# Kernel tuning notes

Measured on AMD Instinct MI355X. Metric: run time of the kernel, lower is better.

Reference implementation:

```python
import jax, jax.numpy as jnp
import numpy as np

_KX = jnp.array([[1., 0., -1.], [2., 0., -2.], [1., 0., -1.]], dtype=jnp.float32).reshape(1, 1, 3, 3)
_KY = jnp.transpose(_KX, (0, 1, 3, 2))  # ky = kx.transpose(2,3)


def _sobel(x, k):
    # x: [B,1,H,W], k: [1,1,3,3]; SAME padding=1, stride 1
    return jax.lax.conv_general_dilated(
        x, k, window_strides=(1, 1), padding=((1, 1), (1, 1)),
        dimension_numbers=('NCHW', 'OIHW', 'NCHW'))


def setup_inputs() -> dict:
    key = jax.random.key(0)
    k1, k2 = jax.random.split(key)
    sr = jax.random.normal(k1, (32, 1, 1024, 1024), dtype=jnp.float32)
    hr = jax.random.normal(k2, (32, 1, 1024, 1024), dtype=jnp.float32)
    return {"sr": sr, "hr": hr}


def reference(sr, hr):
    gx_sr = _sobel(sr, _KX)
    gy_sr = _sobel(sr, _KY)
    gx_hr = _sobel(hr, _KX)
    gy_hr = _sobel(hr, _KY)
    return jnp.mean(jnp.abs(gx_sr - gx_hr) + jnp.abs(gy_sr - gy_hr))
```

## Files before the change

### kernel.cpp

```cpp
#include <hip/hip_runtime.h>


#define IMG_H 1024
#define IMG_W 1024
#define IMG_B 32
#define CH 8
#define NROW (CH + 2)
#define NCHUNK (IMG_H / CH)

#define GLOBAL_PTR(p) ((const __attribute__((address_space(1))) void*)(p))
#define LDS_PTR(p)    ((__attribute__((address_space(3))) void*)(p))

__device__ __forceinline__ void row_st_lds(const float* __restrict__ a,
                                           const float* __restrict__ b,
                                           int x0, float m,
                                           float4& s, float4& t) {
    const float4 av = *reinterpret_cast<const float4*>(a + x0);
    const float4 bv = *reinterpret_cast<const float4*>(b + x0);
    float4 d;
    d.x = (av.x - bv.x) * m;
    d.y = (av.y - bv.y) * m;
    d.z = (av.z - bv.z) * m;
    d.w = (av.w - bv.w) * m;
    const float dl = (x0 > 0)           ? (a[x0 - 1] - b[x0 - 1]) * m : 0.f;
    const float dr = (x0 + 4 < IMG_W)   ? (a[x0 + 4] - b[x0 + 4]) * m : 0.f;
    s.x = dl  + 2.f * d.x + d.y;
    s.y = d.x + 2.f * d.y + d.z;
    s.z = d.y + 2.f * d.z + d.w;
    s.w = d.z + 2.f * d.w + dr;
    t.x = dl  - d.y;
    t.y = d.x - d.z;
    t.z = d.y - d.w;
    t.w = d.z - dr;
}

__global__ __launch_bounds__(256) void edge_loss_kernel(
        const float* __restrict__ sr, const float* __restrict__ hr,
        float* __restrict__ out, float invN) {
    __shared__ __align__(16) float lA[NROW][IMG_W];
    __shared__ __align__(16) float lB[NROW][IMG_W];

    const int chunk = blockIdx.x;
    const int b     = blockIdx.y;
    const int tid   = threadIdx.x;
    const int lane  = tid & 63;
    const int wave  = tid >> 6;
    const int x0    = tid * 4;
    const int wseg  = wave * 256;
    const size_t img = (size_t)b * IMG_H * IMG_W;
    const int y0 = chunk * CH;

    #pragma unroll
    for (int r = 0; r < NROW; ++r) {
        const int yc = min(max(y0 - 1 + r, 0), IMG_H - 1);
        const size_t off = img + (size_t)yc * IMG_W + wseg + lane * 4;
        __builtin_amdgcn_global_load_lds(GLOBAL_PTR(sr + off), LDS_PTR(&lA[r][wseg]), 16, 0, 0);
        __builtin_amdgcn_global_load_lds(GLOBAL_PTR(hr + off), LDS_PTR(&lB[r][wseg]), 16, 0, 0);
    }
    __syncthreads();

    const float mtop = (y0 > 0) ? 1.f : 0.f;
    const float mbot = (y0 + CH < IMG_H) ? 1.f : 0.f;

    float4 s0, t0, s1, t1, s2, t2;
    row_st_lds(lA[0], lB[0], x0, mtop, s0, t0);
    row_st_lds(lA[1], lB[1], x0, 1.f,  s1, t1);

    float acc = 0.f;
    #pragma unroll
    for (int i = 2; i < NROW; ++i) {
        const float m = (i == NROW - 1) ? mbot : 1.f;
        row_st_lds(lA[i], lB[i], x0, m, s2, t2);

        float gx, gy;
        gx = t0.x + 2.f * t1.x + t2.x;  gy = s0.x - s2.x;  acc += fabsf(gx) + fabsf(gy);
        gx = t0.y + 2.f * t1.y + t2.y;  gy = s0.y - s2.y;  acc += fabsf(gx) + fabsf(gy);
        gx = t0.z + 2.f * t1.z + t2.z;  gy = s0.z - s2.z;  acc += fabsf(gx) + fabsf(gy);
        gx = t0.w + 2.f * t1.w + t2.w;  gy = s0.w - s2.w;  acc += fabsf(gx) + fabsf(gy);

        s0 = s1; t0 = t1; s1 = s2; t1 = t2;
    }

    #pragma unroll
    for (int off = 32; off > 0; off >>= 1)
        acc += __shfl_down(acc, off, 64);

    __syncthreads();
    if (lane == 0) lA[0][wave] = acc;
    __syncthreads();
    if (tid == 0) {
        const float bsum = lA[0][0] + lA[0][1] + lA[0][2] + lA[0][3];
        atomicAdd(out, bsum * invN);
    }
}

extern "C" void kernel_launch(void* const* d_in, const int* in_sizes, int n_in,
                              void* d_out, int out_size, void* d_ws, size_t ws_size,
                              hipStream_t stream) {
    const float* sr = (const float*)d_in[0];
    const float* hr = (const float*)d_in[1];
    float* out = (float*)d_out;

    hipMemsetAsync(out, 0, sizeof(float), stream);

    dim3 grid(NCHUNK, IMG_B);
    const float invN = 1.0f / (float)((size_t)IMG_B * IMG_H * IMG_W);
    edge_loss_kernel<<<grid, 256, 0, stream>>>(sr, hr, out, invN);
}
```

Before: 278.3 us.

## Process 64-row strips per block with an LDS ring buffer and prefetching

Each block now handles a 64-row strip in eight 8-row chunks instead of a single chunk. An 18-row LDS ring is filled with global_load_lds, and the next chunk's rows are prefetched while the current one is computed, synchronised with vmcnt waits and barriers. This removes the halo re-reads between chunks and overlaps load latency with compute. In exchange it uses 144KB of LDS per block, allowing about one block per CU, and launches far fewer blocks (512), which risks lower occupancy and idle CUs.

```diff
diff --git a/kernel.cpp b/kernel.cpp
--- a/kernel.cpp
+++ b/kernel.cpp
@@ -5,8 +5,9 @@
 #define IMG_W 1024
 #define IMG_B 32
 #define CH 8
-#define NROW (CH + 2)
-#define NCHUNK (IMG_H / CH)
+#define NCHUNK 8
+#define STRIPS (IMG_H / (CH * NCHUNK))
+#define RING 18
 
 #define GLOBAL_PTR(p) ((const __attribute__((address_space(1))) void*)(p))
 #define LDS_PTR(p)    ((__attribute__((address_space(3))) void*)(p))
@@ -22,8 +23,8 @@
     d.y = (av.y - bv.y) * m;
     d.z = (av.z - bv.z) * m;
     d.w = (av.w - bv.w) * m;
-    const float dl = (x0 > 0)           ? (a[x0 - 1] - b[x0 - 1]) * m : 0.f;
-    const float dr = (x0 + 4 < IMG_W)   ? (a[x0 + 4] - b[x0 + 4]) * m : 0.f;
+    const float dl = (x0 > 0)         ? (a[x0 - 1] - b[x0 - 1]) * m : 0.f;
+    const float dr = (x0 + 4 < IMG_W) ? (a[x0 + 4] - b[x0 + 4]) * m : 0.f;
     s.x = dl  + 2.f * d.x + d.y;
     s.y = d.x + 2.f * d.y + d.z;
     s.z = d.y + 2.f * d.z + d.w;
@@ -37,10 +38,10 @@
 __global__ __launch_bounds__(256) void edge_loss_kernel(
         const float* __restrict__ sr, const float* __restrict__ hr,
         float* __restrict__ out, float invN) {
-    __shared__ __align__(16) float lA[NROW][IMG_W];
-    __shared__ __align__(16) float lB[NROW][IMG_W];
+    __shared__ __align__(16) float lA[RING][IMG_W];
+    __shared__ __align__(16) float lB[RING][IMG_W];
 
-    const int chunk = blockIdx.x;
+    const int strip = blockIdx.x;
     const int b     = blockIdx.y;
     const int tid   = threadIdx.x;
     const int lane  = tid & 63;
@@ -48,37 +49,68 @@
     const int x0    = tid * 4;
     const int wseg  = wave * 256;
     const size_t img = (size_t)b * IMG_H * IMG_W;
-    const int y0 = chunk * CH;
+    const int r0 = strip * (CH * NCHUNK);
+
+    auto stage = [&](int l, int slot) {
+        const int yc = min(max(r0 - 1 + l, 0), IMG_H - 1);
+        const size_t off = img + (size_t)yc * IMG_W + wseg + lane * 4;
+        __builtin_amdgcn_global_load_lds(GLOBAL_PTR(sr + off), LDS_PTR(&lA[slot][wseg]), 16, 0, 0);
+        __builtin_amdgcn_global_load_lds(GLOBAL_PTR(hr + off), LDS_PTR(&lB[slot][wseg]), 16, 0, 0);
+    };
 
     #pragma unroll
-    for (int r = 0; r < NROW; ++r) {
-        const int yc = min(max(y0 - 1 + r, 0), IMG_H - 1);
-        const size_t off = img + (size_t)yc * IMG_W + wseg + lane * 4;
-        __builtin_amdgcn_global_load_lds(GLOBAL_PTR(sr + off), LDS_PTR(&lA[r][wseg]), 16, 0, 0);
-        __builtin_amdgcn_global_load_lds(GLOBAL_PTR(hr + off), LDS_PTR(&lB[r][wseg]), 16, 0, 0);
-    }
-    __syncthreads();
-
-    const float mtop = (y0 > 0) ? 1.f : 0.f;
-    const float mbot = (y0 + CH < IMG_H) ? 1.f : 0.f;
-
-    float4 s0, t0, s1, t1, s2, t2;
-    row_st_lds(lA[0], lB[0], x0, mtop, s0, t0);
-    row_st_lds(lA[1], lB[1], x0, 1.f,  s1, t1);
+    for (int l = 0; l < RING; ++l) stage(l, l);
+    asm volatile("s_waitcnt vmcnt(16)" ::: "memory");
+    __builtin_amdgcn_s_barrier();
 
     float acc = 0.f;
-    #pragma unroll
-    for (int i = 2; i < NROW; ++i) {
-        const float m = (i == NROW - 1) ? mbot : 1.f;
-        row_st_lds(lA[i], lB[i], x0, m, s2, t2);
+    int kb = 0;
 
-        float gx, gy;
-        gx = t0.x + 2.f * t1.x + t2.x;  gy = s0.x - s2.x;  acc += fabsf(gx) + fabsf(gy);
-        gx = t0.y + 2.f * t1.y + t2.y;  gy = s0.y - s2.y;  acc += fabsf(gx) + fabsf(gy);
-        gx = t0.z + 2.f * t1.z + t2.z;  gy = s0.z - s2.z;  acc += fabsf(gx) + fabsf(gy);
-        gx = t0.w + 2.f * t1.w + t2.w;  gy = s0.w - s2.w;  acc += fabsf(gx) + fabsf(gy);
+    for (int k = 0; k < NCHUNK; ++k) {
+        const int yTop = r0 + CH * k;
+        const float mtop = (yTop > 0) ? 1.f : 0.f;
+        const float mbot = (yTop + CH < IMG_H) ? 1.f : 0.f;
 
-        s0 = s1; t0 = t1; s1 = s2; t1 = t2;
+        float4 s0, t0, s1, t1, s2, t2;
+        {
+            int sl0 = kb;
+            int sl1 = kb + 1; if (sl1 >= RING) sl1 -= RING;
+            row_st_lds(lA[sl0], lB[sl0], x0, mtop, s0, t0);
+            row_st_lds(lA[sl1], lB[sl1], x0, 1.f,  s1, t1);
+        }
+        #pragma unroll
+        for (int i = 2; i < CH + 2; ++i) {
+            int sl = kb + i; if (sl >= RING) sl -= RING;
+            const float m = (i == CH + 1) ? mbot : 1.f;
+            row_st_lds(lA[sl], lB[sl], x0, m, s2, t2);
+
+            float gx, gy;
+            gx = t0.x + 2.f * t1.x + t2.x;  gy = s0.x - s2.x;  acc += fabsf(gx) + fabsf(gy);
+            gx = t0.y + 2.f * t1.y + t2.y;  gy = s0.y - s2.y;  acc += fabsf(gx) + fabsf(gy);
+            gx = t0.z + 2.f * t1.z + t2.z;  gy = s0.z - s2.z;  acc += fabsf(gx) + fabsf(gy);
+            gx = t0.w + 2.f * t1.w + t2.w;  gy = s0.w - s2.w;  acc += fabsf(gx) + fabsf(gy);
+
+            s0 = s1; t0 = t1; s1 = s2; t1 = t2;
+        }
+
+        if (k < NCHUNK - 1) {
+            asm volatile("s_waitcnt lgkmcnt(0)" ::: "memory");
+            __builtin_amdgcn_s_barrier();
+
+            if (k < NCHUNK - 2) {
+                #pragma unroll
+                for (int j = 0; j < CH; ++j) {
+                    int sl = kb + j; if (sl >= RING) sl -= RING;
+                    stage(CH * k + RING + j, sl);
+                }
+                asm volatile("s_waitcnt vmcnt(16)" ::: "memory");
+            } else {
+                asm volatile("s_waitcnt vmcnt(0)" ::: "memory");
+            }
+            __builtin_amdgcn_s_barrier();
+        }
+
+        kb += CH; if (kb >= RING) kb -= RING;
     }
 
     #pragma unroll
@@ -103,7 +135,7 @@
 
     hipMemsetAsync(out, 0, sizeof(float), stream);
 
-    dim3 grid(NCHUNK, IMG_B);
+    dim3 grid(STRIPS, IMG_B);
     const float invN = 1.0f / (float)((size_t)IMG_B * IMG_H * IMG_W);
     edge_loss_kernel<<<grid, 256, 0, stream>>>(sr, hr, out, invN);
 }
```

New measurement: 280.4 us. No clear change (+0.8%).

## Replace LDS staging with register double-buffered row loads and shuffle halos

Applied to the files above, without the earlier changes.

The LDS staging through global_load_lds and the block barrier are removed. Each thread now loads its float4 of sr/hr straight into registers, keeping two rows in flight as a rolling prefetch. Horizontal neighbours come from wave shuffles, and only the edge lanes do scalar halo loads. Strips grow from 8 to 16 rows, which cuts the redundant halo-row reads, and the grid is flattened to 1D. The costs are fewer blocks, more registers per thread, and shuffle overhead on every row.

```diff
diff --git a/kernel.cpp b/kernel.cpp
--- a/kernel.cpp
+++ b/kernel.cpp
@@ -4,73 +4,79 @@
 #define IMG_H 1024
 #define IMG_W 1024
 #define IMG_B 32
-#define CH 8
-#define NROW (CH + 2)
-#define NCHUNK (IMG_H / CH)
+#define WROWS 16
+#define NLOAD (WROWS + 2)
+#define RSTRIPS (IMG_H / WROWS)
+#define NBLK (IMG_B * RSTRIPS)
 
-#define GLOBAL_PTR(p) ((const __attribute__((address_space(1))) void*)(p))
-#define LDS_PTR(p)    ((__attribute__((address_space(3))) void*)(p))
-
-__device__ __forceinline__ void row_st_lds(const float* __restrict__ a,
-                                           const float* __restrict__ b,
-                                           int x0, float m,
-                                           float4& s, float4& t) {
-    const float4 av = *reinterpret_cast<const float4*>(a + x0);
-    const float4 bv = *reinterpret_cast<const float4*>(b + x0);
-    float4 d;
-    d.x = (av.x - bv.x) * m;
-    d.y = (av.y - bv.y) * m;
-    d.z = (av.z - bv.z) * m;
-    d.w = (av.w - bv.w) * m;
-    const float dl = (x0 > 0)           ? (a[x0 - 1] - b[x0 - 1]) * m : 0.f;
-    const float dr = (x0 + 4 < IMG_W)   ? (a[x0 + 4] - b[x0 + 4]) * m : 0.f;
-    s.x = dl  + 2.f * d.x + d.y;
-    s.y = d.x + 2.f * d.y + d.z;
-    s.z = d.y + 2.f * d.z + d.w;
-    s.w = d.z + 2.f * d.w + dr;
-    t.x = dl  - d.y;
-    t.y = d.x - d.z;
-    t.z = d.y - d.w;
-    t.w = d.z - dr;
-}
+struct RowBuf { float4 a, b; float ha, hb; };
 
 __global__ __launch_bounds__(256) void edge_loss_kernel(
         const float* __restrict__ sr, const float* __restrict__ hr,
         float* __restrict__ out, float invN) {
-    __shared__ __align__(16) float lA[NROW][IMG_W];
-    __shared__ __align__(16) float lB[NROW][IMG_W];
+    const int tid  = threadIdx.x;
+    const int lane = tid & 63;
+    const int wv   = tid >> 6;
+    const int bidx = blockIdx.x;
+    const int b    = bidx >> 6;
+    const int ys   = bidx & 63;
+    const int y0   = ys * WROWS;
+    const int x0   = wv * 256 + lane * 4;
+    const size_t img = (size_t)b * IMG_H * IMG_W;
 
-    const int chunk = blockIdx.x;
-    const int b     = blockIdx.y;
-    const int tid   = threadIdx.x;
-    const int lane  = tid & 63;
-    const int wave  = tid >> 6;
-    const int x0    = tid * 4;
-    const int wseg  = wave * 256;
-    const size_t img = (size_t)b * IMG_H * IMG_W;
-    const int y0 = chunk * CH;
+    const bool edge = (lane == 0) | (lane == 63);
+    const int  hx   = (lane == 0) ? x0 - 1 : x0 + 4;
+    const float hm  = ((unsigned)hx < IMG_W) ? 1.f : 0.f;
+    const int  hxc  = min(max(hx, 0), IMG_W - 1);
 
-    #pragma unroll
-    for (int r = 0; r < NROW; ++r) {
-        const int yc = min(max(y0 - 1 + r, 0), IMG_H - 1);
-        const size_t off = img + (size_t)yc * IMG_W + wseg + lane * 4;
-        __builtin_amdgcn_global_load_lds(GLOBAL_PTR(sr + off), LDS_PTR(&lA[r][wseg]), 16, 0, 0);
-        __builtin_amdgcn_global_load_lds(GLOBAL_PTR(hr + off), LDS_PTR(&lB[r][wseg]), 16, 0, 0);
-    }
-    __syncthreads();
+    auto LOAD = [&](int l, RowBuf& r) {
+        const int rc = min(max(y0 - 1 + l, 0), IMG_H - 1);
+        const size_t row = img + (size_t)rc * IMG_W;
+        r.a = *reinterpret_cast<const float4*>(sr + row + x0);
+        r.b = *reinterpret_cast<const float4*>(hr + row + x0);
+        if (edge) { r.ha = sr[row + hxc]; r.hb = hr[row + hxc]; }
+        else      { r.ha = 0.f;           r.hb = 0.f;           }
+    };
 
-    const float mtop = (y0 > 0) ? 1.f : 0.f;
-    const float mbot = (y0 + CH < IMG_H) ? 1.f : 0.f;
+    auto ST = [&](const RowBuf& r, float m, float4& s, float4& t) {
+        float4 d;
+        d.x = (r.a.x - r.b.x) * m;
+        d.y = (r.a.y - r.b.y) * m;
+        d.z = (r.a.z - r.b.z) * m;
+        d.w = (r.a.w - r.b.w) * m;
+        const float h = (r.ha - r.hb) * (m * hm);
+        float dl = __shfl_up(d.w, 1);
+        float dr = __shfl_down(d.x, 1);
+        if (lane == 0)  dl = h;
+        if (lane == 63) dr = h;
+        s.x = dl  + 2.f * d.x + d.y;
+        s.y = d.x + 2.f * d.y + d.z;
+        s.z = d.y + 2.f * d.z + d.w;
+        s.w = d.z + 2.f * d.w + dr;
+        t.x = dl  - d.y;
+        t.y = d.x - d.z;
+        t.z = d.y - d.w;
+        t.w = d.z - dr;
+    };
+
+    RowBuf b0, b1;
+    LOAD(0, b0);
+    LOAD(1, b1);
 
     float4 s0, t0, s1, t1, s2, t2;
-    row_st_lds(lA[0], lB[0], x0, mtop, s0, t0);
-    row_st_lds(lA[1], lB[1], x0, 1.f,  s1, t1);
+    const float mT = (y0 > 0) ? 1.f : 0.f;
+    ST(b0, mT, s0, t0);
+    LOAD(2, b0);
+    ST(b1, 1.f, s1, t1);
+    LOAD(3, b1);
 
     float acc = 0.f;
     #pragma unroll
-    for (int i = 2; i < NROW; ++i) {
-        const float m = (i == NROW - 1) ? mbot : 1.f;
-        row_st_lds(lA[i], lB[i], x0, m, s2, t2);
+    for (int i = 0; i < WROWS; ++i) {
+        RowBuf& cur = (i & 1) ? b1 : b0;
+        const float m = ((unsigned)(y0 + i + 1) < IMG_H) ? 1.f : 0.f;
+        ST(cur, m, s2, t2);
+        if (i + 4 < NLOAD) LOAD(i + 4, cur);
 
         float gx, gy;
         gx = t0.x + 2.f * t1.x + t2.x;  gy = s0.x - s2.x;  acc += fabsf(gx) + fabsf(gy);
@@ -85,11 +91,11 @@
     for (int off = 32; off > 0; off >>= 1)
         acc += __shfl_down(acc, off, 64);
 
-    __syncthreads();
-    if (lane == 0) lA[0][wave] = acc;
+    __shared__ float wsum[4];
+    if (lane == 0) wsum[wv] = acc;
     __syncthreads();
     if (tid == 0) {
-        const float bsum = lA[0][0] + lA[0][1] + lA[0][2] + lA[0][3];
+        const float bsum = wsum[0] + wsum[1] + wsum[2] + wsum[3];
         atomicAdd(out, bsum * invN);
     }
 }
@@ -103,7 +109,6 @@
 
     hipMemsetAsync(out, 0, sizeof(float), stream);
 
-    dim3 grid(NCHUNK, IMG_B);
     const float invN = 1.0f / (float)((size_t)IMG_B * IMG_H * IMG_W);
-    edge_loss_kernel<<<grid, 256, 0, stream>>>(sr, hr, out, invN);
+    edge_loss_kernel<<<dim3(NBLK), 256, 0, stream>>>(sr, hr, out, invN);
 }
```

After: 280.5 us. About the same (+0.8%).
